# Optimization experiments

Measured on AMD Instinct MI355X. Metric: run time of the kernel, lower is better.

The kernel has to match this reference:

```python
import jax, jax.numpy as jnp
import numpy as np

ALPHA = 0.3


def _maxsim_scores(q, d):
    # q: [B, N, D], d: [C, S, D] -> scores [B, C]
    # MaxSim: per (query b, doc c), sum over query tokens of max over doc tokens.
    sim = jnp.einsum('bnd,csd->bcns', q, d)  # [B, C, N, S]
    return sim.max(axis=3).sum(axis=2)       # [B, C]


def setup_inputs() -> dict:
    key = jax.random.key(0)
    k1, k2, k3, k4 = jax.random.split(key, 4)
    B, N, S, D = 64, 32, 1024, 128
    return {
        'query_embeddings': jax.random.normal(k1, (B, N, D), dtype=jnp.float32),
        'doc_embeddings': jax.random.normal(k2, (B, S, D), dtype=jnp.float32),
        'teacher_query_outputs': jax.random.normal(k3, (B, N, D), dtype=jnp.float32),
        'teacher_doc_outputs': jax.random.normal(k4, (B, S, D), dtype=jnp.float32),
    }


def reference(query_embeddings, doc_embeddings, teacher_query_outputs, teacher_doc_outputs):
    scores = _maxsim_scores(query_embeddings, doc_embeddings)  # [B, B]
    B = scores.shape[0]
    pos_scores = jnp.diag(scores)                               # [B]
    eye = jnp.eye(B, dtype=bool)
    s_masked = jnp.where(eye, -jnp.inf, scores)
    neg_scores = s_masked.max(axis=1)                           # hardest negative per query
    contrastive_loss = jax.nn.softplus(neg_scores - pos_scores).mean()

    teacher_scores = _maxsim_scores(teacher_query_outputs, teacher_doc_outputs)
    # Torch MSELoss on fp16-cast inputs: compute in fp16, then promote.
    diff16 = scores.astype(jnp.float16) - teacher_scores.astype(jnp.float16)
    mse_loss = jnp.mean(diff16 * diff16).astype(jnp.float32)

    return contrastive_loss + ALPHA * mse_loss
```

## Files before the change

### kernel.cpp

```cpp
#include <hip/hip_runtime.h>
#include <hip/hip_bf16.h>

typedef __attribute__((ext_vector_type(8))) short short8;
typedef __attribute__((ext_vector_type(4))) float floatx4;

#define B_SZ   64
#define N_TOK  32
#define S_TOK  1024
#define D_DIM  128
#define ALPHA  0.3f

#define STRIP_S     32
#define STRIP_EL    (STRIP_S * D_DIM)
#define STRIP_BYTES (STRIP_EL * 2)
#define NSTRIP      (S_TOK / STRIP_S)
#define C_EL        (S_TOK * D_DIM)

#define DBLK (B_SZ * S_TOK * D_DIM / 8 / 256)
#define QBLK (B_SZ * N_TOK * D_DIM / 8 / 256)

__device__ __forceinline__ short f2bf(float f) {
    __hip_bfloat16 h = __float2bfloat16(f);
    return __builtin_bit_cast(short, h);
}

__device__ __forceinline__ short8 cvt8(const float* __restrict__ p) {
    floatx4 f0 = *reinterpret_cast<const floatx4*>(p);
    floatx4 f1 = *reinterpret_cast<const floatx4*>(p + 4);
    short8 r;
    r[0] = f2bf(f0[0]); r[1] = f2bf(f0[1]); r[2] = f2bf(f0[2]); r[3] = f2bf(f0[3]);
    r[4] = f2bf(f1[0]); r[5] = f2bf(f1[1]); r[6] = f2bf(f1[2]); r[7] = f2bf(f1[3]);
    return r;
}

__global__ __launch_bounds__(256) void cvt_all_kernel(
    const float* __restrict__ q,  const float* __restrict__ d,
    const float* __restrict__ tq, const float* __restrict__ td,
    __hip_bfloat16* __restrict__ qb,  __hip_bfloat16* __restrict__ db,
    __hip_bfloat16* __restrict__ tqb, __hip_bfloat16* __restrict__ tdb) {
    const int which = blockIdx.y;
    if (blockIdx.x >= DBLK) {
        const float* src = which ? tq : q;
        __hip_bfloat16* dst = which ? tqb : qb;
        int idx = (blockIdx.x - DBLK) * 256 + threadIdx.x;
        *reinterpret_cast<short8*>(dst + (size_t)idx * 8) = cvt8(src + (size_t)idx * 8);
    } else {
        const float* src = which ? td : d;
        __hip_bfloat16* dst = which ? tdb : db;
        int idx = blockIdx.x * 256 + threadIdx.x;
        int kc = idx & 15;
        int s  = (idx >> 4) & (S_TOK - 1);
        int c  = idx >> 14;
        int st = s >> 5, nt = (s >> 4) & 1, lr = s & 15;
        int ks = kc >> 2, lg = kc & 3;
        size_t dpos = (size_t)c * C_EL + (size_t)st * STRIP_EL
                    + (size_t)(ks * 2 + nt) * 512 + (size_t)(lg * 16 + lr) * 8;
        *reinterpret_cast<short8*>(dst + dpos) = cvt8(src + (size_t)idx * 8);
    }
}

__global__ __launch_bounds__(256, 2) void maxsim_scores_kernel(
    const __hip_bfloat16* __restrict__ qb,  const __hip_bfloat16* __restrict__ db,
    const __hip_bfloat16* __restrict__ tqb, const __hip_bfloat16* __restrict__ tdb,
    float* __restrict__ scores_ws ) {

    const int c     = blockIdx.x;
    const int bg    = blockIdx.y;
    const int which = blockIdx.z;
    const __hip_bfloat16* Q = which ? tqb : qb;
    const __hip_bfloat16* D = which ? tdb : db;
    float* out = scores_ws + which * (B_SZ * B_SZ);

    const int tid = threadIdx.x;
    const int w   = tid >> 6;
    const int l   = tid & 63;
    const int lg  = l >> 4;
    const int lr  = l & 15;

    const int b0 = bg * 16 + w * 4;

    short8 afrag[8][4];
#pragma unroll
    for (int mt = 0; mt < 8; ++mt)
#pragma unroll
        for (int ks = 0; ks < 4; ++ks)
            afrag[mt][ks] = *reinterpret_cast<const short8*>(
                Q + ((size_t)(b0 + (mt >> 1)) * N_TOK + (mt & 1) * 16 + lr) * D_DIM
                  + ks * 32 + lg * 8);
#pragma unroll
    for (int mt = 0; mt < 8; ++mt)
#pragma unroll
        for (int ks = 0; ks < 4; ++ks)
            asm volatile("" : "+v"(afrag[mt][ks]));

    float runmax[8][4];
#pragma unroll
    for (int mt = 0; mt < 8; ++mt)
#pragma unroll
        for (int j = 0; j < 4; ++j) runmax[mt][j] = -INFINITY;

    const char* gbase = (const char*)(D + (size_t)c * C_EL) + l * 16;

    auto load_phase = [&](short8 bb[4], int st, int nt) {
        const char* p = gbase + (size_t)st * STRIP_BYTES + nt * 1024;
#pragma unroll
        for (int ks = 0; ks < 4; ++ks)
            bb[ks] = *reinterpret_cast<const short8*>(p + ks * 2048);
    };

    auto compute = [&](const short8 bb[4]) {
        floatx4 acc[8];
#pragma unroll
        for (int mt = 0; mt < 8; ++mt) acc[mt] = floatx4{0.f, 0.f, 0.f, 0.f};
#pragma unroll
        for (int ks = 0; ks < 4; ++ks)
#pragma unroll
            for (int mt = 0; mt < 8; ++mt)
                acc[mt] = __builtin_amdgcn_mfma_f32_16x16x32_bf16(
                    afrag[mt][ks], bb[ks], acc[mt], 0, 0, 0);
#pragma unroll
        for (int mt = 0; mt < 8; ++mt)
#pragma unroll
            for (int j = 0; j < 4; ++j)
                runmax[mt][j] = fmaxf(runmax[mt][j], acc[mt][j]);
    };

    short8 bb0[4], bb1[4];
    load_phase(bb0, 0, 0);

    for (int st = 0; st < NSTRIP - 1; ++st) {
        load_phase(bb1, st, 1);
        compute(bb0);
        load_phase(bb0, st + 1, 0);
        compute(bb1);
    }
    load_phase(bb1, NSTRIP - 1, 1);
    compute(bb0);
    compute(bb1);

#pragma unroll
    for (int mt = 0; mt < 8; ++mt)
#pragma unroll
        for (int j = 0; j < 4; ++j) {
            float v = runmax[mt][j];
            v = fmaxf(v, __shfl_xor(v, 1));
            v = fmaxf(v, __shfl_xor(v, 2));
            v = fmaxf(v, __shfl_xor(v, 4));
            v = fmaxf(v, __shfl_xor(v, 8));
            runmax[mt][j] = v;
        }

#pragma unroll
    for (int p = 0; p < 4; ++p) {
        float s = 0.f;
#pragma unroll
        for (int j = 0; j < 4; ++j) s += runmax[2 * p][j] + runmax[2 * p + 1][j];
        s += __shfl_xor(s, 16);
        s += __shfl_xor(s, 32);
        if (l == 0) out[(b0 + p) * B_SZ + c] = s;
    }
}

__global__ void loss_kernel(const float* __restrict__ scores_ws, float* __restrict__ out) {
    const float* sc = scores_ws;
    const float* tc = scores_ws + B_SZ * B_SZ;
    const int b = threadIdx.x;

    float pos = sc[b * B_SZ + b];
    float neg = -INFINITY;
    float msesum = 0.f;
#pragma unroll 8
    for (int cc = 0; cc < B_SZ; ++cc) {
        float s = sc[b * B_SZ + cc];
        float t = tc[b * B_SZ + cc];
        if (cc != b) neg = fmaxf(neg, s);
        _Float16 d16 = (_Float16)s - (_Float16)t;
        _Float16 sq  = d16 * d16;
        msesum += (float)sq;
    }
    float x = neg - pos;
    float sp = (x > 0.f) ? (x + log1pf(expf(-x))) : log1pf(expf(x));

#pragma unroll
    for (int m = 1; m < 64; m <<= 1) {
        sp     += __shfl_xor(sp, m);
        msesum += __shfl_xor(msesum, m);
    }
    if (b == 0) {
        float mse = msesum / 4096.f;
        mse = (float)(_Float16)mse;
        out[0] = sp / 64.f + ALPHA * mse;
    }
}

extern "C" void kernel_launch(void* const* d_in, const int* in_sizes, int n_in,
                              void* d_out, int out_size, void* d_ws, size_t ws_size,
                              hipStream_t stream) {
    const float* q  = (const float*)d_in[0];
    const float* d  = (const float*)d_in[1];
    const float* tq = (const float*)d_in[2];
    const float* td = (const float*)d_in[3];
    float* out = (float*)d_out;

    const size_t QN = (size_t)B_SZ * N_TOK * D_DIM;
    const size_t DN = (size_t)B_SZ * S_TOK * D_DIM;

    float* scores_ws = (float*)d_ws;
    __hip_bfloat16* qb  = (__hip_bfloat16*)((char*)d_ws + 32768);
    __hip_bfloat16* tqb = qb + QN;
    __hip_bfloat16* db  = tqb + QN;
    __hip_bfloat16* tdb = db + DN;

    cvt_all_kernel<<<dim3(DBLK + QBLK, 2), 256, 0, stream>>>(
        q, d, tq, td, qb, db, tqb, tdb);

    dim3 grid(B_SZ, B_SZ / 16, 2);
    maxsim_scores_kernel<<<grid, 256, 0, stream>>>(qb, db, tqb, tdb, scores_ws);
    loss_kernel<<<1, 64, 0, stream>>>(scores_ws, out);
}
```

Before: 77.59 us.

## Switch maxsim to 32x32x16 MFMA tiles with two queries per wave

The scoring kernel now uses 32x32x16 bf16 MFMA instructions instead of 16x16x32, with each wave covering two queries (32 tokens each) rather than four. The doc conversion layout is rearranged to match the new B-fragment ordering. The grid doubles in the query-group dimension. This trades more blocks and twice the doc reads per query for fewer MFMA issues and a larger per-instruction tile, which may shift the kernel from compute-bound toward memory-bound.

Result: slower. 95.16 us (+22.6%).

```diff
diff --git a/kernel.cpp b/kernel.cpp
--- a/kernel.cpp
+++ b/kernel.cpp
@@ -1,8 +1,9 @@
 #include <hip/hip_runtime.h>
 #include <hip/hip_bf16.h>
 
-typedef __attribute__((ext_vector_type(8))) short short8;
-typedef __attribute__((ext_vector_type(4))) float floatx4;
+typedef __attribute__((ext_vector_type(8)))  short short8;
+typedef __attribute__((ext_vector_type(4)))  float floatx4;
+typedef __attribute__((ext_vector_type(16))) float floatx16;
 
 #define B_SZ   64
 #define N_TOK  32
@@ -48,13 +49,13 @@
         const float* src = which ? td : d;
         __hip_bfloat16* dst = which ? tdb : db;
         int idx = blockIdx.x * 256 + threadIdx.x;
-        int kc = idx & 15;
+        int k8 = idx & 15;
         int s  = (idx >> 4) & (S_TOK - 1);
         int c  = idx >> 14;
-        int st = s >> 5, nt = (s >> 4) & 1, lr = s & 15;
-        int ks = kc >> 2, lg = kc & 3;
+        int st = s >> 5, sl = s & 31;
+        int kt = k8 >> 1, kh = k8 & 1;
         size_t dpos = (size_t)c * C_EL + (size_t)st * STRIP_EL
-                    + (size_t)(ks * 2 + nt) * 512 + (size_t)(lg * 16 + lr) * 8;
+                    + (size_t)kt * 512 + (size_t)(kh * 32 + sl) * 8;
         *reinterpret_cast<short8*>(dst + dpos) = cvt8(src + (size_t)idx * 8);
     }
 }
@@ -71,93 +72,97 @@
     const __hip_bfloat16* D = which ? tdb : db;
     float* out = scores_ws + which * (B_SZ * B_SZ);
 
-    const int tid = threadIdx.x;
-    const int w   = tid >> 6;
-    const int l   = tid & 63;
-    const int lg  = l >> 4;
-    const int lr  = l & 15;
-
-    const int b0 = bg * 16 + w * 4;
-
-    short8 afrag[8][4];
-#pragma unroll
-    for (int mt = 0; mt < 8; ++mt)
-#pragma unroll
-        for (int ks = 0; ks < 4; ++ks)
-            afrag[mt][ks] = *reinterpret_cast<const short8*>(
-                Q + ((size_t)(b0 + (mt >> 1)) * N_TOK + (mt & 1) * 16 + lr) * D_DIM
-                  + ks * 32 + lg * 8);
-#pragma unroll
-    for (int mt = 0; mt < 8; ++mt)
-#pragma unroll
-        for (int ks = 0; ks < 4; ++ks)
-            asm volatile("" : "+v"(afrag[mt][ks]));
-
-    float runmax[8][4];
-#pragma unroll
-    for (int mt = 0; mt < 8; ++mt)
-#pragma unroll
-        for (int j = 0; j < 4; ++j) runmax[mt][j] = -INFINITY;
+    const int tid  = threadIdx.x;
+    const int w    = tid >> 6;
+    const int l    = tid & 63;
+    const int row  = l & 31;
+    const int half = l >> 5;
+
+    const int b0 = (bg * 4 + w) * 2;
+
+    short8 afrag[2][8];
+#pragma unroll
+    for (int mt = 0; mt < 2; ++mt)
+#pragma unroll
+        for (int kt = 0; kt < 8; ++kt)
+            afrag[mt][kt] = *reinterpret_cast<const short8*>(
+                Q + ((size_t)(b0 + mt) * N_TOK + row) * D_DIM + kt * 16 + half * 8);
+#pragma unroll
+    for (int mt = 0; mt < 2; ++mt)
+#pragma unroll
+        for (int kt = 0; kt < 8; ++kt)
+            asm volatile("" : "+v"(afrag[mt][kt]));
+
+    floatx16 runmax[2];
+    floatx16 fzero;
+#pragma unroll
+    for (int j = 0; j < 16; ++j) {
+        fzero[j] = 0.f;
+        runmax[0][j] = -INFINITY;
+        runmax[1][j] = -INFINITY;
+    }
 
     const char* gbase = (const char*)(D + (size_t)c * C_EL) + l * 16;
 
-    auto load_phase = [&](short8 bb[4], int st, int nt) {
-        const char* p = gbase + (size_t)st * STRIP_BYTES + nt * 1024;
-#pragma unroll
-        for (int ks = 0; ks < 4; ++ks)
-            bb[ks] = *reinterpret_cast<const short8*>(p + ks * 2048);
+    auto load_strip = [&](short8 (&bb)[8], int st) {
+        const char* p = gbase + (size_t)st * STRIP_BYTES;
+#pragma unroll
+        for (int kt = 0; kt < 8; ++kt)
+            bb[kt] = *reinterpret_cast<const short8*>(p + kt * 1024);
     };
 
-    auto compute = [&](const short8 bb[4]) {
-        floatx4 acc[8];
-#pragma unroll
-        for (int mt = 0; mt < 8; ++mt) acc[mt] = floatx4{0.f, 0.f, 0.f, 0.f};
-#pragma unroll
-        for (int ks = 0; ks < 4; ++ks)
-#pragma unroll
-            for (int mt = 0; mt < 8; ++mt)
-                acc[mt] = __builtin_amdgcn_mfma_f32_16x16x32_bf16(
-                    afrag[mt][ks], bb[ks], acc[mt], 0, 0, 0);
-#pragma unroll
-        for (int mt = 0; mt < 8; ++mt)
-#pragma unroll
-            for (int j = 0; j < 4; ++j)
+    auto compute = [&](const short8 (&bb)[8]) {
+        floatx16 acc[2];
+#pragma unroll
+        for (int mt = 0; mt < 2; ++mt)
+            acc[mt] = __builtin_amdgcn_mfma_f32_32x32x16_bf16(
+                afrag[mt][0], bb[0], fzero, 0, 0, 0);
+#pragma unroll
+        for (int kt = 1; kt < 8; ++kt)
+#pragma unroll
+            for (int mt = 0; mt < 2; ++mt)
+                acc[mt] = __builtin_amdgcn_mfma_f32_32x32x16_bf16(
+                    afrag[mt][kt], bb[kt], acc[mt], 0, 0, 0);
+#pragma unroll
+        for (int mt = 0; mt < 2; ++mt)
+#pragma unroll
+            for (int j = 0; j < 16; ++j)
                 runmax[mt][j] = fmaxf(runmax[mt][j], acc[mt][j]);
     };
 
-    short8 bb0[4], bb1[4];
-    load_phase(bb0, 0, 0);
-
-    for (int st = 0; st < NSTRIP - 1; ++st) {
-        load_phase(bb1, st, 1);
-        compute(bb0);
-        load_phase(bb0, st + 1, 0);
-        compute(bb1);
-    }
-    load_phase(bb1, NSTRIP - 1, 1);
-    compute(bb0);
-    compute(bb1);
-
-#pragma unroll
-    for (int mt = 0; mt < 8; ++mt)
-#pragma unroll
-        for (int j = 0; j < 4; ++j) {
-            float v = runmax[mt][j];
+    short8 bA[8], bB[8];
+    load_strip(bA, 0);
+
+    for (int st = 0; st + 2 < NSTRIP; st += 2) {
+        load_strip(bB, st + 1);
+        compute(bA);
+        load_strip(bA, st + 2);
+        compute(bB);
+    }
+    load_strip(bB, NSTRIP - 1);
+    compute(bA);
+    compute(bB);
+
+#pragma unroll
+    for (int mt = 0; mt < 2; ++mt)
+#pragma unroll
+        for (int r = 0; r < 16; ++r) {
+            float v = runmax[mt][r];
             v = fmaxf(v, __shfl_xor(v, 1));
             v = fmaxf(v, __shfl_xor(v, 2));
             v = fmaxf(v, __shfl_xor(v, 4));
             v = fmaxf(v, __shfl_xor(v, 8));
-            runmax[mt][j] = v;
+            v = fmaxf(v, __shfl_xor(v, 16));
+            runmax[mt][r] = v;
         }
 
 #pragma unroll
-    for (int p = 0; p < 4; ++p) {
+    for (int mt = 0; mt < 2; ++mt) {
         float s = 0.f;
 #pragma unroll
-        for (int j = 0; j < 4; ++j) s += runmax[2 * p][j] + runmax[2 * p + 1][j];
-        s += __shfl_xor(s, 16);
+        for (int r = 0; r < 16; ++r) s += runmax[mt][r];
         s += __shfl_xor(s, 32);
-        if (l == 0) out[(b0 + p) * B_SZ + c] = s;
+        if (l == 0) out[(b0 + mt) * B_SZ + c] = s;
     }
 }
 
@@ -214,7 +219,7 @@
     cvt_all_kernel<<<dim3(DBLK + QBLK, 2), 256, 0, stream>>>(
         q, d, tq, td, qb, db, tqb, tdb);
 
-    dim3 grid(B_SZ, B_SZ / 16, 2);
+    dim3 grid(B_SZ, B_SZ / 8, 2);
     maxsim_scores_kernel<<<grid, 256, 0, stream>>>(qb, db, tqb, tdb, scores_ws);
     loss_kernel<<<1, 64, 0, stream>>>(scores_ws, out);
 }
```
